# Optimization experiments

Hardware: AMD Instinct MI355X
Metric: run time of the kernel (lower is better)

The kernel has to match this reference:

```python
import jax, jax.numpy as jnp
import numpy as np

MASK_VAL = -1e18


def _soft_nn(src, src_mask, tgt, tgt_mask):
    """score[b,i,j] = -mean_d (src[b,i,d]-tgt[b,j,d])^2, masked softmax over j,
    then soft nearest neighbor = weights @ tgt.  Uses the |a|^2+|b|^2-2ab
    expansion instead of materializing the [B,M,N,D] broadcast tensor."""
    D = src.shape[-1]
    sq_s = jnp.sum(src * src, axis=-1)                 # [B,M]
    sq_t = jnp.sum(tgt * tgt, axis=-1)                 # [B,N]
    dots = jnp.einsum('bid,bjd->bij', src, tgt)        # [B,M,N]
    dist = (sq_s[:, :, None] + sq_t[:, None, :] - 2.0 * dots) / D
    valid = (src_mask[:, :, None] > 0) & (tgt_mask[:, None, :] > 0)
    score = jnp.where(valid, -dist, MASK_VAL)
    weights = jax.nn.softmax(score, axis=-1)           # [B,M,N]
    nn = jnp.einsum('bij,bjd->bid', weights, tgt)      # [B,M,D]
    return nn, weights


def _cycle_loss(mask, lens, beta):
    """Expected index under beta vs. original index; only the diagonal of the
    original [B,M,M] distance matrix survives, so compute it directly."""
    M = mask.shape[-1]
    idx = jnp.arange(M, dtype=beta.dtype)              # [M]
    index_nn = jnp.einsum('j,bij->bi', idx, beta)      # [B,M]
    l_seq = jnp.square(index_nn - idx[None, :]) * (mask > 0)  # diag of masked dist
    return jnp.mean(jnp.sum(l_seq, axis=-1) / lens)


def setup_inputs() -> dict:
    key = jax.random.key(0)
    kce, kse, kcl, ksl = jax.random.split(key, 4)
    B, M, N, D = 32, 1024, 1024, 128
    clip_lens = jax.random.randint(kcl, (B,), M // 2, M + 1)
    sent_lens = jax.random.randint(ksl, (B,), N // 2, N + 1)
    # original code requires max(lens) == padded length (idx_orig broadcast)
    clip_lens = clip_lens.at[0].set(M)
    sent_lens = sent_lens.at[0].set(N)
    clip_mask = (jnp.arange(M)[None, :] < clip_lens[:, None]).astype(jnp.float32)
    sent_mask = (jnp.arange(N)[None, :] < sent_lens[:, None]).astype(jnp.float32)
    return {
        'clip_emb': jax.random.normal(kce, (B, M, D), dtype=jnp.float32),
        'clip_mask': clip_mask,
        'clip_lens': clip_lens.astype(jnp.float32),
        'sent_emb': jax.random.normal(kse, (B, N, D), dtype=jnp.float32),
        'sent_mask': sent_mask,
        'sent_lens': sent_lens.astype(jnp.float32),
    }


def reference(clip_emb, clip_mask, clip_lens, sent_emb, sent_mask, sent_lens):
    # clip -> sent -> clip cycle
    clip_sent_nn, _ = _soft_nn(clip_emb, clip_mask, sent_emb, sent_mask)
    _, clip_beta = _soft_nn(clip_sent_nn, clip_mask, clip_emb, clip_mask)
    clip_clip_loss = _cycle_loss(clip_mask, clip_lens, clip_beta)
    # sent -> clip -> sent cycle
    sent_clip_nn, _ = _soft_nn(sent_emb, sent_mask, clip_emb, clip_mask)
    _, sent_beta = _soft_nn(sent_clip_nn, sent_mask, sent_emb, sent_mask)
    sent_sent_loss = _cycle_loss(sent_mask, sent_lens, sent_beta)
    return (clip_clip_loss, sent_sent_loss)
```

## Files before the change

### kernel.cpp

```cpp
#include <hip/hip_runtime.h>
#include <hip/hip_bf16.h>
#include <math.h>

typedef __attribute__((ext_vector_type(16))) float f32x16;
typedef __attribute__((ext_vector_type(8))) short short8;
typedef __attribute__((ext_vector_type(4))) short short4v;
typedef __attribute__((ext_vector_type(4))) unsigned uint4v;

#define BATCH 32
#define SEQ 1024
#define DIM 128
#define NBLK 512
#define TILE_BYTES 16384
#define CDOT 0.02254211097f
#define SQE_SCALE 0.011271055485f

__device__ __forceinline__ float exp2f_fast(float x) {
  float r;
  asm("v_exp_f32 %0, %1" : "=v"(r) : "v"(x));
  return r;
}

__device__ __forceinline__ unsigned cvt_pk_bf16(float lo, float hi) {
  unsigned r;
  asm("v_cvt_pk_bf16_f32 %0, %1, %2" : "=v"(r) : "v"(lo), "v"(hi));
  return r;
}

__device__ __forceinline__ unsigned vs_off(int j, int k) {
  return ((unsigned)(k >> 4) << 11) + ((unsigned)j << 5)
       + ((((unsigned)(k & 15)) << 1) ^ ((((unsigned)j >> 2) & 1) << 4));
}

__device__ __forceinline__ short4v ds_tr16(unsigned addr) {
  short4v r;
  asm volatile("ds_read_b64_tr_b16 %0, %1" : "=v"(r) : "v"(addr));
  return r;
}

typedef __attribute__((address_space(1))) const unsigned int gu32;
typedef __attribute__((address_space(3))) unsigned int lu32;
__device__ __forceinline__ void gload_lds16(const void* g, void* l) {
  __builtin_amdgcn_global_load_lds((gu32*)g, (lu32*)l, 16, 0, 0);
}

__global__ __launch_bounds__(256)
void prepack_kernel(const float* __restrict__ clip, const float* __restrict__ sent,
                    char* __restrict__ outN, float* __restrict__ sqe_all) {
  const int bid = blockIdx.x;
  const int tid = threadIdx.x;
  const float* inp = (bid < NBLK) ? clip : sent;
  const size_t row0 = (size_t)(bid & (NBLK - 1)) * 64;
  char* ot = outN + (size_t)bid * TILE_BYTES;
  #pragma unroll
  for (int it = 0; it < 8; ++it) {
    int idx = it * 256 + tid;
    int j = idx >> 5, q = idx & 31;
    float4 v = *reinterpret_cast<const float4*>(inp + (row0 + j) * DIM + q * 4);
    uint2 pk;
    pk.x = cvt_pk_bf16(v.x, v.y);
    pk.y = cvt_pk_bf16(v.z, v.w);
    *reinterpret_cast<uint2*>(ot + vs_off(j, q * 4)) = pk;
    float s = v.x * v.x + v.y * v.y + v.z * v.z + v.w * v.w;
    #pragma unroll
    for (int off = 1; off < 32; off <<= 1) s += __shfl_xor(s, off);
    if ((tid & 31) == 0) sqe_all[bid * 64 + j] = s * SQE_SCALE;
  }
}

__global__ __launch_bounds__(256)
void cycle_kernel(const char* __restrict__ embN, const float* __restrict__ sqe_all,
                  const float* __restrict__ clip_lens, const float* __restrict__ sent_lens,
                  float* __restrict__ partials)
{
  __shared__ __align__(16) char VS[2][TILE_BYTES];
  __shared__ __align__(16) float SQL[2][SEQ];

  const int tid = threadIdx.x;
  const int x = blockIdx.x;
  const int b   = (x & 7) + 8 * (x >> 6);
  const int mm  = (x >> 3) & 7;
  const int cyc = mm >> 2;
  const int qb  = mm & 3;

  const char* srcN = embN + (cyc ? (size_t)NBLK * TILE_BYTES : 0);
  const char* othN = embN + (cyc ? 0 : (size_t)NBLK * TILE_BYTES);
  const float* sqe_src = sqe_all + (cyc ? BATCH * SEQ : 0) + b * SEQ;
  const float* sqe_oth = sqe_all + (cyc ? 0 : BATCH * SEQ) + b * SEQ;
  const float* lens_src = cyc ? sent_lens : clip_lens;
  const float* lens_oth = cyc ? clip_lens : sent_lens;

  const int w = tid >> 6, l = tid & 63;
  const int il = l & 31, hi = l >> 5, g1 = (l >> 4) & 1;

  const char* src_tiles = srcN + (size_t)(b * 16) * TILE_BYTES;
  const char* oth_tiles = othN + (size_t)(b * 16) * TILE_BYTES;

  const int nv1 = (int)(lens_oth[b] + 0.5f);
  const int nv2 = (int)(lens_src[b] + 0.5f);
  const int nt1 = (nv1 + 63) >> 6;
  const int nt2 = (nv2 + 63) >> 6;

  auto STAGE = [&](int buf, const char* gt) {
    #pragma unroll
    for (int i = 0; i < 4; ++i)
      gload_lds16(gt + i * 4096 + tid * 16, &VS[buf][i * 4096 + tid * 16]);
  };

  STAGE(0, oth_tiles);
  {
    float4 vo = reinterpret_cast<const float4*>(sqe_oth)[tid];
    float4 vq = reinterpret_cast<const float4*>(sqe_src)[tid];
    reinterpret_cast<float4*>(&SQL[0][0])[tid] = vo;
    reinterpret_cast<float4*>(&SQL[1][0])[tid] = vq;
  }

  const unsigned qk0 = (unsigned)(il * 32 + ((hi * 16) ^ (((il >> 2) & 1) << 4)));
  const int t16 = (l & 8) ? -16 : 16;

  short8 aq[2][8];
  {
    const char* qt = src_tiles + (size_t)(qb * 4 + w) * TILE_BYTES;
    #pragma unroll
    for (int s = 0; s < 2; ++s) {
      const unsigned qoff = (unsigned)((s * 32 + il) * 32
                            + ((hi * 16) ^ (((il >> 2) & 1) << 4)));
      #pragma unroll
      for (int kc = 0; kc < 8; ++kc)
        aq[s][kc] = *reinterpret_cast<const short8*>(qt + qoff + kc * 2048);
    }
  }

  f32x16 nn[2][4];
  #pragma unroll
  for (int s = 0; s < 2; ++s)
    #pragma unroll
    for (int d = 0; d < 4; ++d)
      #pragma unroll
      for (int r = 0; r < 16; ++r) nn[s][d][r] = 0.f;
  float lsum[2] = {0.f, 0.f};

  asm volatile("s_waitcnt vmcnt(0)" ::: "memory");
  __syncthreads();

  int cur = 0;
  for (int t = 0; t < nt1; ++t) {
    const int jb = t * 64;
    if (t + 1 < nt1) STAGE(cur ^ 1, oth_tiles + (size_t)(t + 1) * TILE_BYTES);
    else             STAGE(cur ^ 1, src_tiles);

    const char* vsc = &VS[cur][0];
    const unsigned vsb = (unsigned)(size_t)vsc;
    const unsigned trb0 = vsb + (unsigned)(g1 * 1920);
    const unsigned trb1 = trb0 + (unsigned)(128 + t16);
    const bool partial = (jb + 64) > nv1;

    #pragma unroll
    for (int jA = 0; jA < 2; ++jA) {
      f32x16 sa0, sa1;
      #pragma unroll
      for (int r = 0; r < 16; ++r) { sa0[r] = 0.f; sa1[r] = 0.f; }
      #pragma unroll
      for (int kc = 0; kc < 8; ++kc) {
        short8 ka = *reinterpret_cast<const short8*>(vsc + qk0 + jA * 1024 + kc * 2048);
        sa0 = __builtin_amdgcn_mfma_f32_32x32x16_bf16(ka, aq[0][kc], sa0, 0, 0, 0);
        sa1 = __builtin_amdgcn_mfma_f32_32x32x16_bf16(ka, aq[1][kc], sa1, 0, 0, 0);
      }
      #pragma unroll
      for (int q = 0; q < 4; ++q) {
        float4 sq4 = *reinterpret_cast<const float4*>(&SQL[0][jb + jA * 32 + q * 8 + hi * 4]);
        sa0[q*4+0] = exp2f_fast(fmaf(sa0[q*4+0], CDOT, -sq4.x));
        sa0[q*4+1] = exp2f_fast(fmaf(sa0[q*4+1], CDOT, -sq4.y));
        sa0[q*4+2] = exp2f_fast(fmaf(sa0[q*4+2], CDOT, -sq4.z));
        sa0[q*4+3] = exp2f_fast(fmaf(sa0[q*4+3], CDOT, -sq4.w));
        sa1[q*4+0] = exp2f_fast(fmaf(sa1[q*4+0], CDOT, -sq4.x));
        sa1[q*4+1] = exp2f_fast(fmaf(sa1[q*4+1], CDOT, -sq4.y));
        sa1[q*4+2] = exp2f_fast(fmaf(sa1[q*4+2], CDOT, -sq4.z));
        sa1[q*4+3] = exp2f_fast(fmaf(sa1[q*4+3], CDOT, -sq4.w));
      }
      if (partial) {
        #pragma unroll
        for (int r = 0; r < 16; ++r) {
          int j = jb + jA * 32 + (r & 3) + 8 * (r >> 2) + 4 * hi;
          if (j >= nv1) { sa0[r] = 0.f; sa1[r] = 0.f; }
        }
      }
      float ls0 = 0.f, ls1 = 0.f;
      #pragma unroll
      for (int r = 0; r < 16; ++r) { ls0 += sa0[r]; ls1 += sa1[r]; }
      lsum[0] += ls0; lsum[1] += ls1;

      #pragma unroll
      for (int gm = 0; gm < 2; ++gm) {
        const int kap = jA * 2 + gm;
        unsigned a00 = cvt_pk_bf16(sa0[gm*8+0], sa0[gm*8+1]);
        unsigned a01 = cvt_pk_bf16(sa0[gm*8+2], sa0[gm*8+3]);
        unsigned a10 = cvt_pk_bf16(sa0[gm*8+4], sa0[gm*8+5]);
        unsigned a11 = cvt_pk_bf16(sa0[gm*8+6], sa0[gm*8+7]);
        asm volatile("v_permlane32_swap_b32 %0, %1" : "+v"(a00), "+v"(a10));
        asm volatile("v_permlane32_swap_b32 %0, %1" : "+v"(a01), "+v"(a11));
        uint4v pw0; pw0.x = a00; pw0.y = a01; pw0.z = a10; pw0.w = a11;
        short8 paf0 = __builtin_bit_cast(short8, pw0);
        unsigned b00 = cvt_pk_bf16(sa1[gm*8+0], sa1[gm*8+1]);
        unsigned b01 = cvt_pk_bf16(sa1[gm*8+2], sa1[gm*8+3]);
        unsigned b10 = cvt_pk_bf16(sa1[gm*8+4], sa1[gm*8+5]);
        unsigned b11 = cvt_pk_bf16(sa1[gm*8+6], sa1[gm*8+7]);
        asm volatile("v_permlane32_swap_b32 %0, %1" : "+v"(b00), "+v"(b10));
        asm volatile("v_permlane32_swap_b32 %0, %1" : "+v"(b01), "+v"(b11));
        uint4v pw1; pw1.x = b00; pw1.y = b01; pw1.z = b10; pw1.w = b11;
        short8 paf1 = __builtin_bit_cast(short8, pw1);

        short4v t0[4], t1[4];
        #pragma unroll
        for (int dblk = 0; dblk < 4; ++dblk) {
          t0[dblk] = ds_tr16(trb0 + (unsigned)(dblk * 4096 + kap * 512));
          t1[dblk] = ds_tr16(trb1 + (unsigned)(dblk * 4096 + kap * 512));
        }
        asm volatile("s_waitcnt lgkmcnt(0)" ::: "memory");
        __builtin_amdgcn_sched_barrier(0);
        #pragma unroll
        for (int dblk = 0; dblk < 4; ++dblk) {
          short8 vf = __builtin_shufflevector(t0[dblk], t1[dblk], 0, 1, 2, 3, 4, 5, 6, 7);
          nn[0][dblk] = __builtin_amdgcn_mfma_f32_32x32x16_bf16(vf, paf0, nn[0][dblk], 0, 0, 0);
          nn[1][dblk] = __builtin_amdgcn_mfma_f32_32x32x16_bf16(vf, paf1, nn[1][dblk], 0, 0, 0);
        }
      }
    }

    asm volatile("s_waitcnt vmcnt(0)" ::: "memory");
    __syncthreads();
    cur ^= 1;
  }

  short8 aq2[2][8];
  #pragma unroll
  for (int s = 0; s < 2; ++s) {
    lsum[s] += __shfl_xor(lsum[s], 32);
    const float inv1 = 1.f / lsum[s];
    #pragma unroll
    for (int kc = 0; kc < 8; ++kc) {
      const int dblk = kc >> 1, gm = kc & 1;
      unsigned u00 = cvt_pk_bf16(nn[s][dblk][gm*8+0] * inv1, nn[s][dblk][gm*8+1] * inv1);
      unsigned u01 = cvt_pk_bf16(nn[s][dblk][gm*8+2] * inv1, nn[s][dblk][gm*8+3] * inv1);
      unsigned u10 = cvt_pk_bf16(nn[s][dblk][gm*8+4] * inv1, nn[s][dblk][gm*8+5] * inv1);
      unsigned u11 = cvt_pk_bf16(nn[s][dblk][gm*8+6] * inv1, nn[s][dblk][gm*8+7] * inv1);
      asm volatile("v_permlane32_swap_b32 %0, %1" : "+v"(u00), "+v"(u10));
      asm volatile("v_permlane32_swap_b32 %0, %1" : "+v"(u01), "+v"(u11));
      uint4v pw; pw.x = u00; pw.y = u01; pw.z = u10; pw.w = u11;
      aq2[s][kc] = __builtin_bit_cast(short8, pw);
    }
  }

  float l2s[2] = {0.f, 0.f}, ixs[2] = {0.f, 0.f};
  for (int t = 0; t < nt2; ++t) {
    const int jb = t * 64;
    if (t + 1 < nt2) STAGE(cur ^ 1, src_tiles + (size_t)(t + 1) * TILE_BYTES);

    const char* vsc = &VS[cur][0];
    const bool partial = (jb + 64) > nv2;

    #pragma unroll
    for (int jA = 0; jA < 2; ++jA) {
      f32x16 sa0, sa1;
      #pragma unroll
      for (int r = 0; r < 16; ++r) { sa0[r] = 0.f; sa1[r] = 0.f; }
      #pragma unroll
      for (int kc = 0; kc < 8; ++kc) {
        short8 ka = *reinterpret_cast<const short8*>(vsc + qk0 + jA * 1024 + kc * 2048);
        sa0 = __builtin_amdgcn_mfma_f32_32x32x16_bf16(ka, aq2[0][kc], sa0, 0, 0, 0);
        sa1 = __builtin_amdgcn_mfma_f32_32x32x16_bf16(ka, aq2[1][kc], sa1, 0, 0, 0);
      }
      #pragma unroll
      for (int q = 0; q < 4; ++q) {
        float4 sq4 = *reinterpret_cast<const float4*>(&SQL[1][jb + jA * 32 + q * 8 + hi * 4]);
        sa0[q*4+0] = exp2f_fast(fmaf(sa0[q*4+0], CDOT, -sq4.x));
        sa0[q*4+1] = exp2f_fast(fmaf(sa0[q*4+1], CDOT, -sq4.y));
        sa0[q*4+2] = exp2f_fast(fmaf(sa0[q*4+2], CDOT, -sq4.z));
        sa0[q*4+3] = exp2f_fast(fmaf(sa0[q*4+3], CDOT, -sq4.w));
        sa1[q*4+0] = exp2f_fast(fmaf(sa1[q*4+0], CDOT, -sq4.x));
        sa1[q*4+1] = exp2f_fast(fmaf(sa1[q*4+1], CDOT, -sq4.y));
        sa1[q*4+2] = exp2f_fast(fmaf(sa1[q*4+2], CDOT, -sq4.z));
        sa1[q*4+3] = exp2f_fast(fmaf(sa1[q*4+3], CDOT, -sq4.w));
      }
      if (partial) {
        #pragma unroll
        for (int r = 0; r < 16; ++r) {
          int j = jb + jA * 32 + (r & 3) + 8 * (r >> 2) + 4 * hi;
          if (j >= nv2) { sa0[r] = 0.f; sa1[r] = 0.f; }
        }
      }
      #pragma unroll
      for (int r = 0; r < 16; ++r) {
        float jc = (float)(jb + jA * 32 + (r & 3) + 8 * (r >> 2) + 4 * hi);
        l2s[0] += sa0[r];
        l2s[1] += sa1[r];
        ixs[0] = fmaf(sa0[r], jc, ixs[0]);
        ixs[1] = fmaf(sa1[r], jc, ixs[1]);
      }
    }

    asm volatile("s_waitcnt vmcnt(0)" ::: "memory");
    __syncthreads();
    cur ^= 1;
  }

  float acc = 0.f;
  #pragma unroll
  for (int s = 0; s < 2; ++s) {
    l2s[s] += __shfl_xor(l2s[s], 32);
    ixs[s] += __shfl_xor(ixs[s], 32);
    int iabs = qb * 256 + w * 64 + s * 32 + il;
    float diff = ixs[s] / l2s[s] - (float)iabs;
    acc += (iabs < nv2) ? diff * diff : 0.f;
  }
  #pragma unroll
  for (int off = 1; off < 32; off <<= 1) acc += __shfl_xor(acc, off);
  if (l == 0)
    partials[cyc * 512 + (b * 4 + qb) * 4 + w] = acc / ((float)nv2 * (float)BATCH);
}

__global__ void reduce_kernel(const float* __restrict__ partials, float* __restrict__ out) {
  __shared__ float red[256];
  const int c = blockIdx.x;
  float s = 0.f;
  for (int i = threadIdx.x; i < 512; i += 256) s += partials[c * 512 + i];
  red[threadIdx.x] = s;
  __syncthreads();
  for (int off = 128; off > 0; off >>= 1) {
    if (threadIdx.x < off) red[threadIdx.x] += red[threadIdx.x + off];
    __syncthreads();
  }
  if (threadIdx.x == 0) out[c] = red[0];
}

extern "C" void kernel_launch(void* const* d_in, const int* in_sizes, int n_in,
                              void* d_out, int out_size, void* d_ws, size_t ws_size,
                              hipStream_t stream) {
  const float* clip_emb  = (const float*)d_in[0];
  const float* clip_lens = (const float*)d_in[2];
  const float* sent_emb  = (const float*)d_in[3];
  const float* sent_lens = (const float*)d_in[5];
  float* out = (float*)d_out;
  char* wsb = (char*)d_ws;

  char*  embN    = wsb;
  float* sqe_all = (float*)(wsb + 2 * (size_t)NBLK * TILE_BYTES);
  float* parts   = sqe_all + 2 * BATCH * SEQ;

  prepack_kernel<<<2 * NBLK, 256, 0, stream>>>(clip_emb, sent_emb, embN, sqe_all);
  cycle_kernel<<<256, 256, 0, stream>>>(embN, sqe_all, clip_lens, sent_lens, parts);
  reduce_kernel<<<2, 256, 0, stream>>>(parts, out);
}
```

Measured before the change: 80.69 us.

## Split key tiles across wave pairs and double grid to 512 blocks

Each block now handles 128 query rows instead of 256. Pairs of waves share the same query rows and each wave processes half of every 64-key tile, so the grid grows from 256 to 512 blocks and fills more CUs on the device. The partial nn accumulators, softmax sums and index sums of each pair are merged through shared memory after each loop. This costs extra LDS (32KB merge buffer), extra syncthreads and a register-heavy merge, and launch_bounds(256,2) is added to keep two blocks resident per CU.

```diff
diff --git a/kernel.cpp b/kernel.cpp
--- a/kernel.cpp
+++ b/kernel.cpp
@@ -68,20 +68,22 @@
   }
 }
 
-__global__ __launch_bounds__(256)
+__global__ __launch_bounds__(256, 2)
 void cycle_kernel(const char* __restrict__ embN, const float* __restrict__ sqe_all,
                   const float* __restrict__ clip_lens, const float* __restrict__ sent_lens,
                   float* __restrict__ partials)
 {
   __shared__ __align__(16) char VS[2][TILE_BYTES];
   __shared__ __align__(16) float SQL[2][SEQ];
+  __shared__ __align__(16) char MG[32768];
+  __shared__ float RED[4][4][64];
 
   const int tid = threadIdx.x;
   const int x = blockIdx.x;
-  const int b   = (x & 7) + 8 * (x >> 6);
-  const int mm  = (x >> 3) & 7;
-  const int cyc = mm >> 2;
-  const int qb  = mm & 3;
+  const int b   = (x & 7) + 8 * (x >> 7);
+  const int sub = (x >> 3) & 15;
+  const int cyc = sub >> 3;
+  const int qh  = sub & 7;
 
   const char* srcN = embN + (cyc ? (size_t)NBLK * TILE_BYTES : 0);
   const char* othN = embN + (cyc ? 0 : (size_t)NBLK * TILE_BYTES);
@@ -91,6 +93,7 @@
   const float* lens_oth = cyc ? clip_lens : sent_lens;
 
   const int w = tid >> 6, l = tid & 63;
+  const int p = w >> 1, h = w & 1;
   const int il = l & 31, hi = l >> 5, g1 = (l >> 4) & 1;
 
   const char* src_tiles = srcN + (size_t)(b * 16) * TILE_BYTES;
@@ -120,7 +123,7 @@
 
   short8 aq[2][8];
   {
-    const char* qt = src_tiles + (size_t)(qb * 4 + w) * TILE_BYTES;
+    const char* qt = src_tiles + (size_t)(qh * 2 + p) * TILE_BYTES;
     #pragma unroll
     for (int s = 0; s < 2; ++s) {
       const unsigned qoff = (unsigned)((s * 32 + il) * 32
@@ -153,77 +156,74 @@
     const unsigned vsb = (unsigned)(size_t)vsc;
     const unsigned trb0 = vsb + (unsigned)(g1 * 1920);
     const unsigned trb1 = trb0 + (unsigned)(128 + t16);
-    const bool partial = (jb + 64) > nv1;
-
-    #pragma unroll
-    for (int jA = 0; jA < 2; ++jA) {
-      f32x16 sa0, sa1;
-      #pragma unroll
-      for (int r = 0; r < 16; ++r) { sa0[r] = 0.f; sa1[r] = 0.f; }
-      #pragma unroll
-      for (int kc = 0; kc < 8; ++kc) {
-        short8 ka = *reinterpret_cast<const short8*>(vsc + qk0 + jA * 1024 + kc * 2048);
-        sa0 = __builtin_amdgcn_mfma_f32_32x32x16_bf16(ka, aq[0][kc], sa0, 0, 0, 0);
-        sa1 = __builtin_amdgcn_mfma_f32_32x32x16_bf16(ka, aq[1][kc], sa1, 0, 0, 0);
-      }
-      #pragma unroll
-      for (int q = 0; q < 4; ++q) {
-        float4 sq4 = *reinterpret_cast<const float4*>(&SQL[0][jb + jA * 32 + q * 8 + hi * 4]);
-        sa0[q*4+0] = exp2f_fast(fmaf(sa0[q*4+0], CDOT, -sq4.x));
-        sa0[q*4+1] = exp2f_fast(fmaf(sa0[q*4+1], CDOT, -sq4.y));
-        sa0[q*4+2] = exp2f_fast(fmaf(sa0[q*4+2], CDOT, -sq4.z));
-        sa0[q*4+3] = exp2f_fast(fmaf(sa0[q*4+3], CDOT, -sq4.w));
-        sa1[q*4+0] = exp2f_fast(fmaf(sa1[q*4+0], CDOT, -sq4.x));
-        sa1[q*4+1] = exp2f_fast(fmaf(sa1[q*4+1], CDOT, -sq4.y));
-        sa1[q*4+2] = exp2f_fast(fmaf(sa1[q*4+2], CDOT, -sq4.z));
-        sa1[q*4+3] = exp2f_fast(fmaf(sa1[q*4+3], CDOT, -sq4.w));
-      }
-      if (partial) {
-        #pragma unroll
-        for (int r = 0; r < 16; ++r) {
-          int j = jb + jA * 32 + (r & 3) + 8 * (r >> 2) + 4 * hi;
-          if (j >= nv1) { sa0[r] = 0.f; sa1[r] = 0.f; }
-        }
-      }
-      float ls0 = 0.f, ls1 = 0.f;
-      #pragma unroll
-      for (int r = 0; r < 16; ++r) { ls0 += sa0[r]; ls1 += sa1[r]; }
-      lsum[0] += ls0; lsum[1] += ls1;
-
-      #pragma unroll
-      for (int gm = 0; gm < 2; ++gm) {
-        const int kap = jA * 2 + gm;
-        unsigned a00 = cvt_pk_bf16(sa0[gm*8+0], sa0[gm*8+1]);
-        unsigned a01 = cvt_pk_bf16(sa0[gm*8+2], sa0[gm*8+3]);
-        unsigned a10 = cvt_pk_bf16(sa0[gm*8+4], sa0[gm*8+5]);
-        unsigned a11 = cvt_pk_bf16(sa0[gm*8+6], sa0[gm*8+7]);
-        asm volatile("v_permlane32_swap_b32 %0, %1" : "+v"(a00), "+v"(a10));
-        asm volatile("v_permlane32_swap_b32 %0, %1" : "+v"(a01), "+v"(a11));
-        uint4v pw0; pw0.x = a00; pw0.y = a01; pw0.z = a10; pw0.w = a11;
-        short8 paf0 = __builtin_bit_cast(short8, pw0);
-        unsigned b00 = cvt_pk_bf16(sa1[gm*8+0], sa1[gm*8+1]);
-        unsigned b01 = cvt_pk_bf16(sa1[gm*8+2], sa1[gm*8+3]);
-        unsigned b10 = cvt_pk_bf16(sa1[gm*8+4], sa1[gm*8+5]);
-        unsigned b11 = cvt_pk_bf16(sa1[gm*8+6], sa1[gm*8+7]);
-        asm volatile("v_permlane32_swap_b32 %0, %1" : "+v"(b00), "+v"(b10));
-        asm volatile("v_permlane32_swap_b32 %0, %1" : "+v"(b01), "+v"(b11));
-        uint4v pw1; pw1.x = b00; pw1.y = b01; pw1.z = b10; pw1.w = b11;
-        short8 paf1 = __builtin_bit_cast(short8, pw1);
-
-        short4v t0[4], t1[4];
-        #pragma unroll
-        for (int dblk = 0; dblk < 4; ++dblk) {
-          t0[dblk] = ds_tr16(trb0 + (unsigned)(dblk * 4096 + kap * 512));
-          t1[dblk] = ds_tr16(trb1 + (unsigned)(dblk * 4096 + kap * 512));
-        }
-        asm volatile("s_waitcnt lgkmcnt(0)" ::: "memory");
-        __builtin_amdgcn_sched_barrier(0);
-        #pragma unroll
-        for (int dblk = 0; dblk < 4; ++dblk) {
-          short8 vf = __builtin_shufflevector(t0[dblk], t1[dblk], 0, 1, 2, 3, 4, 5, 6, 7);
-          nn[0][dblk] = __builtin_amdgcn_mfma_f32_32x32x16_bf16(vf, paf0, nn[0][dblk], 0, 0, 0);
-          nn[1][dblk] = __builtin_amdgcn_mfma_f32_32x32x16_bf16(vf, paf1, nn[1][dblk], 0, 0, 0);
-        }
+    const bool partial = (jb + h * 32 + 32) > nv1;
+
+    f32x16 sa0, sa1;
+    #pragma unroll
+    for (int r = 0; r < 16; ++r) { sa0[r] = 0.f; sa1[r] = 0.f; }
+    #pragma unroll
+    for (int kc = 0; kc < 8; ++kc) {
+      short8 ka = *reinterpret_cast<const short8*>(vsc + qk0 + h * 1024 + kc * 2048);
+      sa0 = __builtin_amdgcn_mfma_f32_32x32x16_bf16(ka, aq[0][kc], sa0, 0, 0, 0);
+      sa1 = __builtin_amdgcn_mfma_f32_32x32x16_bf16(ka, aq[1][kc], sa1, 0, 0, 0);
+    }
+    #pragma unroll
+    for (int q = 0; q < 4; ++q) {
+      float4 sq4 = *reinterpret_cast<const float4*>(&SQL[0][jb + h * 32 + q * 8 + hi * 4]);
+      sa0[q*4+0] = exp2f_fast(fmaf(sa0[q*4+0], CDOT, -sq4.x));
+      sa0[q*4+1] = exp2f_fast(fmaf(sa0[q*4+1], CDOT, -sq4.y));
+      sa0[q*4+2] = exp2f_fast(fmaf(sa0[q*4+2], CDOT, -sq4.z));
+      sa0[q*4+3] = exp2f_fast(fmaf(sa0[q*4+3], CDOT, -sq4.w));
+      sa1[q*4+0] = exp2f_fast(fmaf(sa1[q*4+0], CDOT, -sq4.x));
+      sa1[q*4+1] = exp2f_fast(fmaf(sa1[q*4+1], CDOT, -sq4.y));
+      sa1[q*4+2] = exp2f_fast(fmaf(sa1[q*4+2], CDOT, -sq4.z));
+      sa1[q*4+3] = exp2f_fast(fmaf(sa1[q*4+3], CDOT, -sq4.w));
+    }
+    if (partial) {
+      #pragma unroll
+      for (int r = 0; r < 16; ++r) {
+        int j = jb + h * 32 + (r & 3) + 8 * (r >> 2) + 4 * hi;
+        if (j >= nv1) { sa0[r] = 0.f; sa1[r] = 0.f; }
+      }
+    }
+    float ls0 = 0.f, ls1 = 0.f;
+    #pragma unroll
+    for (int r = 0; r < 16; ++r) { ls0 += sa0[r]; ls1 += sa1[r]; }
+    lsum[0] += ls0; lsum[1] += ls1;
+
+    #pragma unroll
+    for (int gm = 0; gm < 2; ++gm) {
+      const int kap = h * 2 + gm;
+      unsigned a00 = cvt_pk_bf16(sa0[gm*8+0], sa0[gm*8+1]);
+      unsigned a01 = cvt_pk_bf16(sa0[gm*8+2], sa0[gm*8+3]);
+      unsigned a10 = cvt_pk_bf16(sa0[gm*8+4], sa0[gm*8+5]);
+      unsigned a11 = cvt_pk_bf16(sa0[gm*8+6], sa0[gm*8+7]);
+      asm volatile("v_permlane32_swap_b32 %0, %1" : "+v"(a00), "+v"(a10));
+      asm volatile("v_permlane32_swap_b32 %0, %1" : "+v"(a01), "+v"(a11));
+      uint4v pw0; pw0.x = a00; pw0.y = a01; pw0.z = a10; pw0.w = a11;
+      short8 paf0 = __builtin_bit_cast(short8, pw0);
+      unsigned b00 = cvt_pk_bf16(sa1[gm*8+0], sa1[gm*8+1]);
+      unsigned b01 = cvt_pk_bf16(sa1[gm*8+2], sa1[gm*8+3]);
+      unsigned b10 = cvt_pk_bf16(sa1[gm*8+4], sa1[gm*8+5]);
+      unsigned b11 = cvt_pk_bf16(sa1[gm*8+6], sa1[gm*8+7]);
+      asm volatile("v_permlane32_swap_b32 %0, %1" : "+v"(b00), "+v"(b10));
+      asm volatile("v_permlane32_swap_b32 %0, %1" : "+v"(b01), "+v"(b11));
+      uint4v pw1; pw1.x = b00; pw1.y = b01; pw1.z = b10; pw1.w = b11;
+      short8 paf1 = __builtin_bit_cast(short8, pw1);
+
+      short4v t0[4], t1[4];
+      #pragma unroll
+      for (int dblk = 0; dblk < 4; ++dblk) {
+        t0[dblk] = ds_tr16(trb0 + (unsigned)(dblk * 4096 + kap * 512));
+        t1[dblk] = ds_tr16(trb1 + (unsigned)(dblk * 4096 + kap * 512));
+      }
+      asm volatile("s_waitcnt lgkmcnt(0)" ::: "memory");
+      __builtin_amdgcn_sched_barrier(0);
+      #pragma unroll
+      for (int dblk = 0; dblk < 4; ++dblk) {
+        short8 vf = __builtin_shufflevector(t0[dblk], t1[dblk], 0, 1, 2, 3, 4, 5, 6, 7);
+        nn[0][dblk] = __builtin_amdgcn_mfma_f32_32x32x16_bf16(vf, paf0, nn[0][dblk], 0, 0, 0);
+        nn[1][dblk] = __builtin_amdgcn_mfma_f32_32x32x16_bf16(vf, paf1, nn[1][dblk], 0, 0, 0);
       }
     }
 
@@ -231,6 +231,39 @@
     __syncthreads();
     cur ^= 1;
   }
+
+  RED[w][0][l] = lsum[0];
+  RED[w][1][l] = lsum[1];
+  #pragma unroll
+  for (int c = 0; c < 4; ++c) {
+    const int s = c >> 1, d0 = (c & 1) * 2;
+    #pragma unroll
+    for (int hf = 0; hf < 2; ++hf) {
+      const f32x16 v = nn[s][d0 + hf];
+      #pragma unroll
+      for (int i = 0; i < 4; ++i) {
+        float4 f4;
+        f4.x = v[i*4+0]; f4.y = v[i*4+1]; f4.z = v[i*4+2]; f4.w = v[i*4+3];
+        *reinterpret_cast<float4*>(MG + w * 8192 + (hf * 4 + i) * 1024 + l * 16) = f4;
+      }
+    }
+    __syncthreads();
+    #pragma unroll
+    for (int hf = 0; hf < 2; ++hf) {
+      #pragma unroll
+      for (int i = 0; i < 4; ++i) {
+        float4 f4 = *reinterpret_cast<const float4*>(
+            MG + (w ^ 1) * 8192 + (hf * 4 + i) * 1024 + l * 16);
+        nn[s][d0+hf][i*4+0] += f4.x;
+        nn[s][d0+hf][i*4+1] += f4.y;
+        nn[s][d0+hf][i*4+2] += f4.z;
+        nn[s][d0+hf][i*4+3] += f4.w;
+      }
+    }
+    __syncthreads();
+  }
+  lsum[0] += RED[w ^ 1][0][l];
+  lsum[1] += RED[w ^ 1][1][l];
 
   short8 aq2[2][8];
   #pragma unroll
@@ -257,66 +290,69 @@
     if (t + 1 < nt2) STAGE(cur ^ 1, src_tiles + (size_t)(t + 1) * TILE_BYTES);
 
     const char* vsc = &VS[cur][0];
-    const bool partial = (jb + 64) > nv2;
-
-    #pragma unroll
-    for (int jA = 0; jA < 2; ++jA) {
-      f32x16 sa0, sa1;
-      #pragma unroll
-      for (int r = 0; r < 16; ++r) { sa0[r] = 0.f; sa1[r] = 0.f; }
-      #pragma unroll
-      for (int kc = 0; kc < 8; ++kc) {
-        short8 ka = *reinterpret_cast<const short8*>(vsc + qk0 + jA * 1024 + kc * 2048);
-        sa0 = __builtin_amdgcn_mfma_f32_32x32x16_bf16(ka, aq2[0][kc], sa0, 0, 0, 0);
-        sa1 = __builtin_amdgcn_mfma_f32_32x32x16_bf16(ka, aq2[1][kc], sa1, 0, 0, 0);
-      }
-      #pragma unroll
-      for (int q = 0; q < 4; ++q) {
-        float4 sq4 = *reinterpret_cast<const float4*>(&SQL[1][jb + jA * 32 + q * 8 + hi * 4]);
-        sa0[q*4+0] = exp2f_fast(fmaf(sa0[q*4+0], CDOT, -sq4.x));
-        sa0[q*4+1] = exp2f_fast(fmaf(sa0[q*4+1], CDOT, -sq4.y));
-        sa0[q*4+2] = exp2f_fast(fmaf(sa0[q*4+2], CDOT, -sq4.z));
-        sa0[q*4+3] = exp2f_fast(fmaf(sa0[q*4+3], CDOT, -sq4.w));
-        sa1[q*4+0] = exp2f_fast(fmaf(sa1[q*4+0], CDOT, -sq4.x));
-        sa1[q*4+1] = exp2f_fast(fmaf(sa1[q*4+1], CDOT, -sq4.y));
-        sa1[q*4+2] = exp2f_fast(fmaf(sa1[q*4+2], CDOT, -sq4.z));
-        sa1[q*4+3] = exp2f_fast(fmaf(sa1[q*4+3], CDOT, -sq4.w));
-      }
-      if (partial) {
-        #pragma unroll
-        for (int r = 0; r < 16; ++r) {
-          int j = jb + jA * 32 + (r & 3) + 8 * (r >> 2) + 4 * hi;
-          if (j >= nv2) { sa0[r] = 0.f; sa1[r] = 0.f; }
-        }
-      }
+    const bool partial = (jb + h * 32 + 32) > nv2;
+
+    f32x16 sa0, sa1;
+    #pragma unroll
+    for (int r = 0; r < 16; ++r) { sa0[r] = 0.f; sa1[r] = 0.f; }
+    #pragma unroll
+    for (int kc = 0; kc < 8; ++kc) {
+      short8 ka = *reinterpret_cast<const short8*>(vsc + qk0 + h * 1024 + kc * 2048);
+      sa0 = __builtin_amdgcn_mfma_f32_32x32x16_bf16(ka, aq2[0][kc], sa0, 0, 0, 0);
+      sa1 = __builtin_amdgcn_mfma_f32_32x32x16_bf16(ka, aq2[1][kc], sa1, 0, 0, 0);
+    }
+    #pragma unroll
+    for (int q = 0; q < 4; ++q) {
+      float4 sq4 = *reinterpret_cast<const float4*>(&SQL[1][jb + h * 32 + q * 8 + hi * 4]);
+      sa0[q*4+0] = exp2f_fast(fmaf(sa0[q*4+0], CDOT, -sq4.x));
+      sa0[q*4+1] = exp2f_fast(fmaf(sa0[q*4+1], CDOT, -sq4.y));
+      sa0[q*4+2] = exp2f_fast(fmaf(sa0[q*4+2], CDOT, -sq4.z));
+      sa0[q*4+3] = exp2f_fast(fmaf(sa0[q*4+3], CDOT, -sq4.w));
+      sa1[q*4+0] = exp2f_fast(fmaf(sa1[q*4+0], CDOT, -sq4.x));
+      sa1[q*4+1] = exp2f_fast(fmaf(sa1[q*4+1], CDOT, -sq4.y));
+      sa1[q*4+2] = exp2f_fast(fmaf(sa1[q*4+2], CDOT, -sq4.z));
+      sa1[q*4+3] = exp2f_fast(fmaf(sa1[q*4+3], CDOT, -sq4.w));
+    }
+    if (partial) {
       #pragma unroll
       for (int r = 0; r < 16; ++r) {
-        float jc = (float)(jb + jA * 32 + (r & 3) + 8 * (r >> 2) + 4 * hi);
-        l2s[0] += sa0[r];
-        l2s[1] += sa1[r];
-        ixs[0] = fmaf(sa0[r], jc, ixs[0]);
-        ixs[1] = fmaf(sa1[r], jc, ixs[1]);
-      }
+        int j = jb + h * 32 + (r & 3) + 8 * (r >> 2) + 4 * hi;
+        if (j >= nv2) { sa0[r] = 0.f; sa1[r] = 0.f; }
+      }
+    }
+    #pragma unroll
+    for (int r = 0; r < 16; ++r) {
+      float jc = (float)(jb + h * 32 + (r & 3) + 8 * (r >> 2) + 4 * hi);
+      l2s[0] += sa0[r];
+      l2s[1] += sa1[r];
+      ixs[0] = fmaf(sa0[r], jc, ixs[0]);
+      ixs[1] = fmaf(sa1[r], jc, ixs[1]);
     }
 
     asm volatile("s_waitcnt vmcnt(0)" ::: "memory");
     __syncthreads();
     cur ^= 1;
   }
+
+  RED[w][0][l] = l2s[0]; RED[w][1][l] = l2s[1];
+  RED[w][2][l] = ixs[0]; RED[w][3][l] = ixs[1];
+  __syncthreads();
+  l2s[0] += RED[w ^ 1][0][l]; l2s[1] += RED[w ^ 1][1][l];
+  ixs[0] += RED[w ^ 1][2][l]; ixs[1] += RED[w ^ 1][3][l];
 
   float acc = 0.f;
   #pragma unroll
   for (int s = 0; s < 2; ++s) {
     l2s[s] += __shfl_xor(l2s[s], 32);
     ixs[s] += __shfl_xor(ixs[s], 32);
-    int iabs = qb * 256 + w * 64 + s * 32 + il;
+    int iabs = qh * 128 + p * 64 + s * 32 + il;
     float diff = ixs[s] / l2s[s] - (float)iabs;
     acc += (iabs < nv2) ? diff * diff : 0.f;
   }
   #pragma unroll
   for (int off = 1; off < 32; off <<= 1) acc += __shfl_xor(acc, off);
-  if (l == 0)
-    partials[cyc * 512 + (b * 4 + qb) * 4 + w] = acc / ((float)nv2 * (float)BATCH);
+  if (h == 0 && l == 0)
+    partials[cyc * 512 + (b * 8 + qh) * 2 + p] = acc / ((float)nv2 * (float)BATCH);
 }
 
 __global__ void reduce_kernel(const float* __restrict__ partials, float* __restrict__ out) {
@@ -348,6 +384,6 @@
   float* parts   = sqe_all + 2 * BATCH * SEQ;
 
   prepack_kernel<<<2 * NBLK, 256, 0, stream>>>(clip_emb, sent_emb, embN, sqe_all);
-  cycle_kernel<<<256, 256, 0, stream>>>(embN, sqe_all, clip_lens, sent_lens, parts);
+  cycle_kernel<<<512, 256, 0, stream>>>(embN, sqe_all, clip_lens, sent_lens, parts);
   reduce_kernel<<<2, 256, 0, stream>>>(parts, out);
 }
```

New measurement: 67.98 us. 1.19x faster.
